# Performance work log

Hardware: AMD Instinct MI355X
Metric: run time of the kernel (lower is better)

The kernel has to match this reference:

```python
import jax, jax.numpy as jnp
import numpy as np

D_MODEL = 1024
D_STATE = 16
D_CONV = 4
EXPAND = 2
HEADDIM = 64
NGROUPS = 1
D_INNER = EXPAND * D_MODEL            # 2048
NHEADS = D_INNER // HEADDIM           # 32
CONV_DIM = D_INNER + 2 * NGROUPS * D_STATE   # 2080
D_IN_PROJ = 2 * D_INNER + 2 * NGROUPS * D_STATE + NHEADS  # 4160
EPS = 1e-5
BATCH, SEQLEN = 4, 2048


def setup_inputs() -> dict:
    key = jax.random.key(0)
    ks = jax.random.split(key, 8)
    x = jax.random.normal(ks[0], (BATCH, SEQLEN, D_MODEL), jnp.float32)
    W_in = jax.random.normal(ks[1], (D_MODEL, D_IN_PROJ), jnp.float32) * 0.02
    conv_w = jax.random.normal(ks[2], (CONV_DIM, D_CONV), jnp.float32) * 0.2
    conv_b = jnp.zeros((CONV_DIM,), jnp.float32)
    # dt_bias = inverse softplus of dt drawn in [1e-3, 1e-1] (mamba_ssm init)
    dt = jax.random.uniform(ks[3], (NHEADS,), jnp.float32, 0.001, 0.1)
    dt_bias = jnp.log(jnp.expm1(dt))
    A_log = jnp.log(jax.random.uniform(ks[4], (NHEADS,), jnp.float32, 1.0, 16.0))
    D_param = jnp.ones((NHEADS,), jnp.float32)
    norm_w = jnp.ones((D_INNER,), jnp.float32)
    W_out = jax.random.normal(ks[5], (D_INNER, D_MODEL), jnp.float32) * 0.02
    layer_scale = jnp.full((D_MODEL,), 1e-4, jnp.float32)
    return dict(x=x, W_in=W_in, conv_w=conv_w, conv_b=conv_b, dt_bias=dt_bias,
                A_log=A_log, D_param=D_param, norm_w=norm_w, W_out=W_out,
                layer_scale=layer_scale)


def _silu(v):
    return v * jax.nn.sigmoid(v)


def _mamba2(x, W_in, conv_w, conv_b, dt_bias, A_log, D_param, norm_w, W_out):
    b, l, _ = x.shape
    zxbcdt = x @ W_in                                  # (b, l, d_in_proj)
    z = zxbcdt[..., :D_INNER]                          # gate
    xBC = zxbcdt[..., D_INNER:D_INNER + CONV_DIM]
    dt = jax.nn.softplus(zxbcdt[..., D_INNER + CONV_DIM:] + dt_bias)  # (b, l, h)
    # causal depthwise conv1d (kernel D_CONV) + SiLU
    xp = jnp.pad(xBC, ((0, 0), (D_CONV - 1, 0), (0, 0)))
    conv = sum(xp[:, k:k + l, :] * conv_w[:, k] for k in range(D_CONV)) + conv_b
    xBC = _silu(conv)
    xs = xBC[..., :D_INNER].reshape(b, l, NHEADS, HEADDIM)  # (b, l, h, p)
    Bm = xBC[..., D_INNER:D_INNER + D_STATE]                # (b, l, n), ngroups=1
    Cm = xBC[..., D_INNER + D_STATE:]                       # (b, l, n)
    A = -jnp.exp(A_log)                                     # (h,)
    dA = jnp.exp(dt * A)                                    # (b, l, h)
    dtx = dt[..., None] * xs                                # (b, l, h, p)

    def step(h, inp):
        dA_t, dtx_t, B_t, C_t = inp
        # h: (b, h, p, n)
        h = h * dA_t[..., None, None] + dtx_t[..., None] * B_t[:, None, None, :]
        y = jnp.einsum('bhpn,bn->bhp', h, C_t)
        return h, y

    h0 = jnp.zeros((b, NHEADS, HEADDIM, D_STATE), x.dtype)
    _, ys = jax.lax.scan(step, h0, (dA.transpose(1, 0, 2), dtx.transpose(1, 0, 2, 3),
                                    Bm.transpose(1, 0, 2), Cm.transpose(1, 0, 2)))
    y = ys.transpose(1, 0, 2, 3) + D_param[None, None, :, None] * xs  # (b, l, h, p)
    y = y.reshape(b, l, D_INNER)
    # gated RMSNorm (norm_before_gate=False): gate first, then rmsnorm
    y = y * _silu(z)
    y = y * jax.lax.rsqrt(jnp.mean(y * y, axis=-1, keepdims=True) + EPS) * norm_w
    return y @ W_out


def reference(x, W_in, conv_w, conv_b, dt_bias, A_log, D_param, norm_w, W_out, layer_scale):
    # dropout is identity (eval / p=0)
    return x + _mamba2(x, W_in, conv_w, conv_b, dt_bias, A_log, D_param, norm_w, W_out) * layer_scale
```

## Files before the change

### kernel.cpp

```cpp
#include <hip/hip_runtime.h>
#include <hip/hip_bf16.h>

#define D_MODEL   1024
#define D_STATE   16
#define D_CONV    4
#define HEADDIM   64
#define NHEADS    32
#define D_INNER   2048
#define CONV_DIM  2080
#define D_IN_PROJ 4160
#define NPAD      4224
#define BATCH     4
#define SEQLEN    2048
#define MROWS     (BATCH*SEQLEN)
#define QCHUNK    64
#define NCHUNK    (SEQLEN/QCHUNK)
#define DT_COL    (2*D_INNER + 2*D_STATE)

#define WSCALE    16.f
#define YSCALE    64.f

__device__ __forceinline__ unsigned short f2b(float f) {
    union { float f; unsigned int u; } v; v.f = f;
    unsigned int r = (v.u + 0x7FFFu + ((v.u >> 16) & 1u)) >> 16;
    return (unsigned short)r;
}
__device__ __forceinline__ float b2f(unsigned short h) {
    union { unsigned int u; float f; } v; v.u = ((unsigned int)h) << 16;
    return v.f;
}
__device__ __forceinline__ unsigned char f2fp8(float f) {
    return (unsigned char)(__builtin_amdgcn_cvt_pk_fp8_f32(f, 0.f, 0, false) & 0xFF);
}

typedef __attribute__((ext_vector_type(8))) short bf16x8;
typedef __attribute__((ext_vector_type(4))) float f32x4;
typedef __attribute__((ext_vector_type(4))) int   i32x4;
typedef __attribute__((ext_vector_type(8))) int   i32x8;

__device__ __forceinline__ i32x8 cat8(i32x4 a, i32x4 b) {
    i32x8 r;
    r[0] = a[0]; r[1] = a[1]; r[2] = a[2]; r[3] = a[3];
    r[4] = b[0]; r[5] = b[1]; r[6] = b[2]; r[7] = b[3];
    return r;
}

__device__ __forceinline__ void async_copy16b(const unsigned char* g, unsigned char* l) {
    __builtin_amdgcn_global_load_lds(
        (const __attribute__((address_space(1))) void*)g,
        (__attribute__((address_space(3))) void*)l, 16, 0, 0);
}

__global__ void cast_f32_fp8(const float* __restrict__ in, unsigned char* __restrict__ out, int n) {
    int i = (blockIdx.x * blockDim.x + threadIdx.x) * 4;
    if (i >= n) return;
    float4 v = *(const float4*)&in[i];
    int p = __builtin_amdgcn_cvt_pk_fp8_f32(v.x, v.y, 0, false);
    p = __builtin_amdgcn_cvt_pk_fp8_f32(v.z, v.w, p, true);
    *(unsigned int*)&out[i] = (unsigned int)p;
}

__global__ void transpose_both(const float* __restrict__ W_in, unsigned char* __restrict__ winT,
                               const float* __restrict__ W_out, unsigned char* __restrict__ woutT,
                               const float* __restrict__ norm_w) {
    __shared__ float tile[64][65];
    int bid = blockIdx.x;
    const float* W; unsigned char* WT; const float* kscale;
    int K, N, bx, by;
    if (bid < 1056) { W = W_in;  WT = winT;  kscale = nullptr; K = 1024; N = 4160; bx = bid % 66; by = bid / 66; }
    else { bid -= 1056; W = W_out; WT = woutT; kscale = norm_w; K = 2048; N = 1024; bx = bid % 16; by = bid / 16; }
    int n0 = bx * 64, k0 = by * 64;
    int tx = threadIdx.x & 63, ty = threadIdx.x >> 6;
    #pragma unroll
    for (int i = 0; i < 16; i++) {
        int r = ty * 16 + i;
        int n = n0 + tx;
        float v = (n < N) ? W[(size_t)(k0 + r) * N + n] : 0.f;
        tile[r][tx] = v;
    }
    __syncthreads();
    float ks = WSCALE * (kscale ? kscale[k0 + tx] : 1.f);
    #pragma unroll
    for (int i = 0; i < 16; i++) {
        int r = ty * 16 + i;
        WT[(size_t)(n0 + r) * K + k0 + tx] = f2fp8(tile[tx][r] * ks);
    }
}

template <int EPI>
__global__ __launch_bounds__(256)
void gemm_fp8(const unsigned char* __restrict__ A, const unsigned char* __restrict__ B,
              int K, int N, unsigned short* __restrict__ Cb,
              float* __restrict__ Cf, const float* __restrict__ xres,
              const float* __restrict__ ls, const float* __restrict__ rs) {
    __shared__ unsigned char lds_a[128 * 128];
    __shared__ unsigned char lds_b[128 * 128];
    const int tid  = threadIdx.x;
    const int wave = tid >> 6;
    const int lane = tid & 63;
    const int bid = blockIdx.x;
    const int xcd = bid & 7, g = bid >> 3;
    const int bm = xcd * 8 + (g & 7);
    const int bn = g >> 3;
    const int wm = wave >> 1, wn = wave & 1;

    f32x4 acc[4][4];
    #pragma unroll
    for (int i = 0; i < 4; i++)
        #pragma unroll
        for (int j = 0; j < 4; j++) acc[i][j] = (f32x4){0.f, 0.f, 0.f, 0.f};

    const int srow = lane >> 3;
    const int sseg = (lane & 7) ^ srow;
    const unsigned char* gA0 = A + (size_t)(bm * 128 + wave * 8 + srow) * K + sseg * 16;
    const unsigned char* gB0 = B + (size_t)(bn * 128 + wave * 8 + srow) * K + sseg * 16;
    const int ldsbase = wave * 8 * 128;

    const int lm = lane & 15, q = lane >> 4;

    for (int k0 = 0; k0 < K; k0 += 128) {
        #pragma unroll
        for (int j = 0; j < 4; j++) {
            async_copy16b(gA0 + k0 + (size_t)(j * 32) * K, &lds_a[ldsbase + j * 32 * 128]);
            async_copy16b(gB0 + k0 + (size_t)(j * 32) * K, &lds_b[ldsbase + j * 32 * 128]);
        }
        __syncthreads();

        i32x8 af[4], bfr[4];
        #pragma unroll
        for (int i = 0; i < 4; i++) {
            int r = wm * 64 + i * 16 + lm;
            int s0 = ((2 * q) ^ (r & 7)) * 16, s1 = ((2 * q + 1) ^ (r & 7)) * 16;
            af[i] = cat8(*(const i32x4*)&lds_a[r * 128 + s0],
                         *(const i32x4*)&lds_a[r * 128 + s1]);
        }
        #pragma unroll
        for (int j = 0; j < 4; j++) {
            int r = wn * 64 + j * 16 + lm;
            int s0 = ((2 * q) ^ (r & 7)) * 16, s1 = ((2 * q + 1) ^ (r & 7)) * 16;
            bfr[j] = cat8(*(const i32x4*)&lds_b[r * 128 + s0],
                          *(const i32x4*)&lds_b[r * 128 + s1]);
        }
        #pragma unroll
        for (int i = 0; i < 4; i++)
            #pragma unroll
            for (int j = 0; j < 4; j++)
                acc[i][j] = __builtin_amdgcn_mfma_scale_f32_16x16x128_f8f6f4(
                    af[i], bfr[j], acc[i][j], 0, 0,
                    0, 0x7F7F7F7F, 0, 0x7F7F7F7F);
        __syncthreads();
    }

    const int row0 = bm * 128 + wm * 64;
    const int col0 = bn * 128 + wn * 64;
    const int lq = (lane >> 4) * 4;
    #pragma unroll
    for (int i = 0; i < 4; i++) {
        #pragma unroll
        for (int j = 0; j < 4; j++) {
            #pragma unroll
            for (int r = 0; r < 4; r++) {
                int gr = row0 + i * 16 + lq + r;
                int gc = col0 + j * 16 + lm;
                float v = acc[i][j][r];
                if (EPI == 0) {
                    Cb[(size_t)gr * N + gc] = f2b(v * (1.f / WSCALE));
                } else {
                    size_t idx = (size_t)gr * 1024 + gc;
                    Cf[idx] = xres[idx] + v * ls[gc] * rs[gr] * (1.f / (WSCALE * YSCALE));
                }
            }
        }
    }
}

__global__ __launch_bounds__(256)
void ssd_hcomp(const unsigned short* __restrict__ zx, const float* __restrict__ dt_bias,
               const float* __restrict__ conv_w, const float* __restrict__ conv_b,
               const float* __restrict__ A_log,
               float* __restrict__ hbuf, float* __restrict__ pbuf) {
    __shared__ unsigned short sXraw[67 * 64];
    __shared__ unsigned short sBraw[67 * 32];
    __shared__ unsigned short sXT[64 * 72];
    __shared__ unsigned short sBwT[16 * 72];
    __shared__ float sdt[64], scd[64];

    const int blk = blockIdx.x;
    const int c  = blk & 31;
    const int h  = (blk >> 5) & 31;
    const int b  = blk >> 10;
    const int bh = blk >> 5;
    const int row0 = b * SEQLEN + c * QCHUNK;
    const int batch0 = b * SEQLEN;

    const int t    = threadIdx.x;
    const int w    = t >> 6;
    const int lane = t & 63;
    const int lm   = lane & 15;
    const int lq8  = (lane >> 4) * 8;
    const int lq4  = (lane >> 4) * 4;
    const float Ah = -__expf(A_log[h]);

    for (int i = t; i < 536; i += 256) {
        int r = i >> 3, seg = i & 7;
        int gr = row0 - 3 + r;
        int4 v = (gr >= batch0) ? *(const int4*)&zx[(size_t)gr * NPAD + D_INNER + h * 64 + seg * 8]
                                : (int4){0, 0, 0, 0};
        *(int4*)&sXraw[r * 64 + seg * 8] = v;
    }
    for (int i = t; i < 268; i += 256) {
        int r = i >> 2, seg = i & 3;
        int gr = row0 - 3 + r;
        int4 v = (gr >= batch0) ? *(const int4*)&zx[(size_t)gr * NPAD + 2 * D_INNER + seg * 8]
                                : (int4){0, 0, 0, 0};
        *(int4*)&sBraw[r * 32 + seg * 8] = v;
    }
    if (t < 64) {
        float raw = b2f(zx[(size_t)(row0 + t) * NPAD + DT_COL + h]) + dt_bias[h];
        float dtv = (raw > 20.f) ? raw : log1pf(__expf(raw));
        float v = dtv;
        #pragma unroll
        for (int o = 1; o < 64; o <<= 1) {
            float u = __shfl_up(v, o, 64);
            if (t >= o) v += u;
        }
        sdt[t] = dtv;
        scd[t] = v;
        if (t == 63) pbuf[bh * NCHUNK + c] = __expf(Ah * v);
    }
    __syncthreads();

    {
        const int p = t & 63, sblk = (t >> 6) * 16;
        const int ch = h * 64 + p;
        const float cw0 = conv_w[ch * 4 + 0], cw1 = conv_w[ch * 4 + 1];
        const float cw2 = conv_w[ch * 4 + 2], cw3 = conv_w[ch * 4 + 3];
        const float cb = conv_b[ch];
        #pragma unroll
        for (int i = 0; i < 16; i++) {
            int s = sblk + i;
            float acc = cb + cw0 * b2f(sXraw[s * 64 + p]) + cw1 * b2f(sXraw[(s + 1) * 64 + p])
                           + cw2 * b2f(sXraw[(s + 2) * 64 + p]) + cw3 * b2f(sXraw[(s + 3) * 64 + p]);
            float sv = acc / (1.f + __expf(-acc));
            sXT[p * 72 + s] = f2b(sv);
        }
    }
    {
        const int n = t & 15, s0 = (t >> 4) * 4;
        const int ch = D_INNER + n;
        const float cw0 = conv_w[ch * 4 + 0], cw1 = conv_w[ch * 4 + 1];
        const float cw2 = conv_w[ch * 4 + 2], cw3 = conv_w[ch * 4 + 3];
        const float cb = conv_b[ch];
        const float cdl = scd[63];
        #pragma unroll
        for (int i = 0; i < 4; i++) {
            int s = s0 + i;
            float acc = cb + cw0 * b2f(sBraw[s * 32 + n]) + cw1 * b2f(sBraw[(s + 1) * 32 + n])
                           + cw2 * b2f(sBraw[(s + 2) * 32 + n]) + cw3 * b2f(sBraw[(s + 3) * 32 + n]);
            float sv = acc / (1.f + __expf(-acc));
            float wgt = sdt[s] * __expf(Ah * (cdl - scd[s]));
            sBwT[n * 72 + s] = f2b(sv * wgt);
        }
    }
    __syncthreads();

    f32x4 hacc = (f32x4){0.f, 0.f, 0.f, 0.f};
    #pragma unroll
    for (int ks = 0; ks < 2; ks++) {
        bf16x8 af = *(const bf16x8*)&sBwT[lm * 72 + ks * 32 + lq8];
        bf16x8 bf_ = *(const bf16x8*)&sXT[(w * 16 + lm) * 72 + ks * 32 + lq8];
        hacc = __builtin_amdgcn_mfma_f32_16x16x32_bf16(af, bf_, hacc, 0, 0, 0);
    }
    #pragma unroll
    for (int r = 0; r < 4; r++)
        hbuf[(size_t)(bh * NCHUNK + c) * 1024 + (lq4 + r) * 64 + (w * 16 + lm)] = hacc[r];
}

__global__ __launch_bounds__(1024)
void ssd_state_scan(float* __restrict__ hbuf, const float* __restrict__ pbuf) {
    int bh = blockIdx.x;
    int t = threadIdx.x;
    __shared__ float sP[NCHUNK];
    if (t < NCHUNK) sP[t] = pbuf[bh * NCHUNK + t];
    __syncthreads();
    size_t base = (size_t)bh * NCHUNK * 1024 + t;
    float v[NCHUNK];
    #pragma unroll
    for (int c = 0; c < NCHUNK; c++) v[c] = hbuf[base + (size_t)c * 1024];
    float carry = 0.f;
    #pragma unroll
    for (int c = 0; c < NCHUNK; c++) {
        float tmp = v[c];
        v[c] = carry;
        carry = tmp + sP[c] * carry;
    }
    #pragma unroll
    for (int c = 0; c < NCHUNK; c++) hbuf[base + (size_t)c * 1024] = v[c];
}

__global__ __launch_bounds__(256)
void ssd_yfused(const unsigned short* __restrict__ zx, const float* __restrict__ dt_bias,
                const float* __restrict__ conv_w, const float* __restrict__ conv_b,
                const float* __restrict__ A_log, const float* __restrict__ D_param,
                const float* __restrict__ hbuf,
                unsigned char* __restrict__ y, float* __restrict__ ssq) {
    __shared__ unsigned short sXraw[67 * 64];
    __shared__ unsigned short sBCraw[67 * 32];
    __shared__ unsigned short sB[64 * 32];
    __shared__ unsigned short sC[64 * 32];
    __shared__ unsigned short sXT[64 * 72];
    __shared__ unsigned short sM[64 * 72];
    __shared__ unsigned short sHT[64 * 40];
    __shared__ float sdt[64], scd[64], sSc[64];

    const int blk = blockIdx.x;
    const int c  = blk & 31;
    const int h  = (blk >> 5) & 31;
    const int b  = blk >> 10;
    const int bh = blk >> 5;
    const int row0 = b * SEQLEN + c * QCHUNK;
    const int batch0 = b * SEQLEN;

    const int t    = threadIdx.x;
    const int w    = t >> 6;
    const int lane = t & 63;
    const int lm   = lane & 15;
    const int lq8  = (lane >> 4) * 8;
    const int lq4  = (lane >> 4) * 4;
    const float Ah = -__expf(A_log[h]);

    for (int i = t; i < 536; i += 256) {
        int r = i >> 3, seg = i & 7;
        int gr = row0 - 3 + r;
        int4 v = (gr >= batch0) ? *(const int4*)&zx[(size_t)gr * NPAD + D_INNER + h * 64 + seg * 8]
                                : (int4){0, 0, 0, 0};
        *(int4*)&sXraw[r * 64 + seg * 8] = v;
    }
    for (int i = t; i < 268; i += 256) {
        int r = i >> 2, seg = i & 3;
        int gr = row0 - 3 + r;
        int4 v = (gr >= batch0) ? *(const int4*)&zx[(size_t)gr * NPAD + 2 * D_INNER + seg * 8]
                                : (int4){0, 0, 0, 0};
        *(int4*)&sBCraw[r * 32 + seg * 8] = v;
    }
    {
        size_t hb = (size_t)(bh * NCHUNK + c) * 1024 + (size_t)t * 4;
        float4 hv = *(const float4*)&hbuf[hb];
        int n = t >> 4;
        int p0 = (t * 4) & 63;
        sHT[(p0 + 0) * 40 + n] = f2b(hv.x);
        sHT[(p0 + 1) * 40 + n] = f2b(hv.y);
        sHT[(p0 + 2) * 40 + n] = f2b(hv.z);
        sHT[(p0 + 3) * 40 + n] = f2b(hv.w);
    }
    if (t < 64) {
        float raw = b2f(zx[(size_t)(row0 + t) * NPAD + DT_COL + h]) + dt_bias[h];
        float dtv = (raw > 20.f) ? raw : log1pf(__expf(raw));
        float v = dtv;
        #pragma unroll
        for (int o = 1; o < 64; o <<= 1) {
            float u = __shfl_up(v, o, 64);
            if (t >= o) v += u;
        }
        sdt[t] = dtv;
        scd[t] = v;
        sSc[t] = __expf(Ah * v);
    } else if (t < 128) {
        int tt = t - 64;
        *(int4*)&sHT[tt * 40 + 16] = (int4){0, 0, 0, 0};
        *(int4*)&sHT[tt * 40 + 24] = (int4){0, 0, 0, 0};
    }
    __syncthreads();

    {
        const int p = t & 63, sblk = (t >> 6) * 16;
        const int ch = h * 64 + p;
        const float cw0 = conv_w[ch * 4 + 0], cw1 = conv_w[ch * 4 + 1];
        const float cw2 = conv_w[ch * 4 + 2], cw3 = conv_w[ch * 4 + 3];
        const float cb = conv_b[ch];
        #pragma unroll
        for (int i = 0; i < 16; i++) {
            int s = sblk + i;
            float acc = cb + cw0 * b2f(sXraw[s * 64 + p]) + cw1 * b2f(sXraw[(s + 1) * 64 + p])
                           + cw2 * b2f(sXraw[(s + 2) * 64 + p]) + cw3 * b2f(sXraw[(s + 3) * 64 + p]);
            float sv = acc / (1.f + __expf(-acc));
            sXT[p * 72 + s] = f2b(sv);
        }
    }
    {
        const int ch32 = t & 31, s0 = (t >> 5) * 8;
        const int ch = D_INNER + ch32;
        const float cw0 = conv_w[ch * 4 + 0], cw1 = conv_w[ch * 4 + 1];
        const float cw2 = conv_w[ch * 4 + 2], cw3 = conv_w[ch * 4 + 3];
        const float cb = conv_b[ch];
        unsigned short* dst = (ch32 < 16) ? &sB[ch32] : &sC[ch32 - 16];
        #pragma unroll
        for (int i = 0; i < 8; i++) {
            int s = s0 + i;
            float acc = cb + cw0 * b2f(sBCraw[s * 32 + ch32]) + cw1 * b2f(sBCraw[(s + 1) * 32 + ch32])
                           + cw2 * b2f(sBCraw[(s + 2) * 32 + ch32]) + cw3 * b2f(sBCraw[(s + 3) * 32 + ch32]);
            float sv = acc / (1.f + __expf(-acc));
            dst[s * 32] = f2b(sv);
        }
    }
    if (t < 64) {
        *(int4*)&sB[t * 32 + 16] = (int4){0, 0, 0, 0};
        *(int4*)&sB[t * 32 + 24] = (int4){0, 0, 0, 0};
        *(int4*)&sC[t * 32 + 16] = (int4){0, 0, 0, 0};
        *(int4*)&sC[t * 32 + 24] = (int4){0, 0, 0, 0};
    }
    __syncthreads();

    f32x4 sacc[4];
    {
        bf16x8 cfrag = *(const bf16x8*)&sC[(w * 16 + lm) * 32 + lq8];
        #pragma unroll
        for (int sb = 0; sb < 4; sb++) {
            if (sb <= w) {
                bf16x8 bfrag = *(const bf16x8*)&sB[(sb * 16 + lm) * 32 + lq8];
                sacc[sb] = __builtin_amdgcn_mfma_f32_16x16x32_bf16(
                    cfrag, bfrag, (f32x4){0.f, 0.f, 0.f, 0.f}, 0, 0, 0);
            }
        }
    }
    #pragma unroll
    for (int sb = 0; sb < 4; sb++) {
        int sp = sb * 16 + lm;
        if (sb > w) {
            #pragma unroll
            for (int r = 0; r < 4; r++) sM[(w * 16 + lq4 + r) * 72 + sp] = 0;
        } else {
            float dts = sdt[sp], cds = scd[sp];
            #pragma unroll
            for (int r = 0; r < 4; r++) {
                int tp = w * 16 + lq4 + r;
                float m = 0.f;
                if (sb < w || sp <= tp)
                    m = sacc[sb][r] * dts * __expf(Ah * (scd[tp] - cds));
                sM[tp * 72 + sp] = f2b(m);
            }
        }
    }

    f32x4 yacc[4];
    #pragma unroll
    for (int pb = 0; pb < 4; pb++) yacc[pb] = (f32x4){0.f, 0.f, 0.f, 0.f};
    #pragma unroll
    for (int ks = 0; ks < 2; ks++) {
        if (ks == 1 && w < 2) continue;
        bf16x8 af = *(const bf16x8*)&sM[(w * 16 + lm) * 72 + ks * 32 + lq8];
        #pragma unroll
        for (int pb = 0; pb < 4; pb++) {
            bf16x8 bf_ = *(const bf16x8*)&sXT[(pb * 16 + lm) * 72 + ks * 32 + lq8];
            yacc[pb] = __builtin_amdgcn_mfma_f32_16x16x32_bf16(af, bf_, yacc[pb], 0, 0, 0);
        }
    }
    f32x4 acc2[4];
    {
        bf16x8 cf2 = *(const bf16x8*)&sC[(w * 16 + lm) * 32 + lq8];
        #pragma unroll
        for (int pb = 0; pb < 4; pb++) {
            bf16x8 hf = *(const bf16x8*)&sHT[(pb * 16 + lm) * 40 + lq8];
            acc2[pb] = __builtin_amdgcn_mfma_f32_16x16x32_bf16(
                cf2, hf, (f32x4){0.f, 0.f, 0.f, 0.f}, 0, 0, 0);
        }
    }

    const float Dh = D_param[h];
    #pragma unroll
    for (int r = 0; r < 4; r++) {
        const int tp = w * 16 + lq4 + r;
        const size_t zrow = (size_t)(row0 + tp) * NPAD + h * 64;
        const size_t yrow = (size_t)(row0 + tp) * D_INNER + h * 64;
        float ssr = 0.f;
        #pragma unroll
        for (int pb = 0; pb < 4; pb++) {
            int pp = pb * 16 + lm;
            float xv = b2f(sXT[pp * 72 + tp]);
            float val = yacc[pb][r] + sSc[tp] * acc2[pb][r] + Dh * xv;
            float zv = b2f(zx[zrow + pp]);
            float yg = val * (zv / (1.f + __expf(-zv)));
            ssr += yg * yg;
            y[yrow + pp] = f2fp8(yg * YSCALE);
        }
        ssr += __shfl_xor(ssr, 1, 16);
        ssr += __shfl_xor(ssr, 2, 16);
        ssr += __shfl_xor(ssr, 4, 16);
        ssr += __shfl_xor(ssr, 8, 16);
        if (lm == 0)
            ssq[(size_t)(row0 + tp) * NHEADS + h] = ssr;
    }
}

__global__ __launch_bounds__(256)
void rowscale_kernel(const float* __restrict__ ssq, float* __restrict__ rs) {
    int row = blockIdx.x * 256 + threadIdx.x;
    const float4* p = (const float4*)&ssq[(size_t)row * NHEADS];
    float s = 0.f;
    #pragma unroll
    for (int i = 0; i < 8; i++) {
        float4 v = p[i];
        s += v.x + v.y + v.z + v.w;
    }
    rs[row] = rsqrtf(s * (1.f / D_INNER) + 1e-5f);
}

extern "C" void kernel_launch(void* const* d_in, const int* in_sizes, int n_in,
                              void* d_out, int out_size, void* d_ws, size_t ws_size,
                              hipStream_t stream) {
    const float* x        = (const float*)d_in[0];
    const float* W_in     = (const float*)d_in[1];
    const float* conv_w   = (const float*)d_in[2];
    const float* conv_b   = (const float*)d_in[3];
    const float* dt_bias  = (const float*)d_in[4];
    const float* A_log    = (const float*)d_in[5];
    const float* D_param  = (const float*)d_in[6];
    const float* norm_w   = (const float*)d_in[7];
    const float* W_out    = (const float*)d_in[8];
    const float* ls       = (const float*)d_in[9];
    float* out = (float*)d_out;

    char* ws = (char*)d_ws;
    size_t off = 0;
    unsigned char*  x_f8  = (unsigned char*)(ws + off);  off += (size_t)MROWS * D_MODEL;
    unsigned char*  winT  = (unsigned char*)(ws + off);  off += (size_t)NPAD * D_MODEL;
    unsigned char*  woutT = (unsigned char*)(ws + off);  off += (size_t)D_MODEL * D_INNER;
    unsigned short* zx    = (unsigned short*)(ws + off); off += (size_t)MROWS * NPAD * 2;
    float*          pbuf  = (float*)(ws + off);          off += (size_t)BATCH * NHEADS * NCHUNK * 4;
    unsigned char*  yb    = (unsigned char*)(ws + off);  off += (size_t)MROWS * D_INNER;
    float*          ssq   = (float*)(ws + off);          off += (size_t)MROWS * NHEADS * 4;
    float*          rsb   = (float*)(ws + off);          off += (size_t)MROWS * 4;
    float*          hbuf  = (float*)(ws + off);          off += (size_t)BATCH * NHEADS * NCHUNK * 1024 * 4;

    cast_f32_fp8<<<(MROWS * D_MODEL) / 1024, 256, 0, stream>>>(x, x_f8, MROWS * D_MODEL);
    transpose_both<<<1568, 256, 0, stream>>>(W_in, winT, W_out, woutT, norm_w);
    gemm_fp8<0><<<(NPAD / 128) * 64, 256, 0, stream>>>(
        x_f8, winT, D_MODEL, NPAD, zx, nullptr, nullptr, nullptr, nullptr);
    ssd_hcomp<<<BATCH * NHEADS * NCHUNK, 256, 0, stream>>>(
        zx, dt_bias, conv_w, conv_b, A_log, hbuf, pbuf);
    ssd_state_scan<<<BATCH * NHEADS, 1024, 0, stream>>>(hbuf, pbuf);
    ssd_yfused<<<BATCH * NHEADS * NCHUNK, 256, 0, stream>>>(
        zx, dt_bias, conv_w, conv_b, A_log, D_param, hbuf, yb, ssq);
    rowscale_kernel<<<MROWS / 256, 256, 0, stream>>>(ssq, rsb);
    gemm_fp8<1><<<(D_MODEL / 128) * 64, 256, 0, stream>>>(
        yb, woutT, D_INNER, D_MODEL, nullptr, out, x, ls, rsb);
}
```

Measured before the change: 276.5 us.

## Reuse conv and dt results from hcomp in yfused via global buffers

ssd_hcomp now writes the post-conv SiLU x (already transposed), the B/C conv outputs and the dt, cumsum and decay scalars to workspace buffers, and ssd_yfused reads them instead of recomputing the causal conv, softplus and prefix scan. The D skip term is folded into the diagonal of the intra-chunk matrix, z is staged through shared memory with coalesced loads, and the conv loops reuse a register sliding window. This removes duplicated conv and exp work and the halo loads in the second kernel. The cost is extra global writes and reads of about 32 MB of bf16 x data plus small side buffers, and folding D into bf16 M adds some rounding.

```diff
diff --git a/kernel.cpp b/kernel.cpp
--- a/kernel.cpp
+++ b/kernel.cpp
@@ -178,10 +178,13 @@
 void ssd_hcomp(const unsigned short* __restrict__ zx, const float* __restrict__ dt_bias,
                const float* __restrict__ conv_w, const float* __restrict__ conv_b,
                const float* __restrict__ A_log,
-               float* __restrict__ hbuf, float* __restrict__ pbuf) {
+               float* __restrict__ hbuf, float* __restrict__ pbuf,
+               unsigned short* __restrict__ xTg, unsigned short* __restrict__ bcg,
+               float* __restrict__ scA) {
     __shared__ unsigned short sXraw[67 * 64];
-    __shared__ unsigned short sBraw[67 * 32];
+    __shared__ unsigned short sBCraw[67 * 32];
     __shared__ unsigned short sXT[64 * 72];
+    __shared__ unsigned short sBC[64 * 32];
     __shared__ unsigned short sBwT[16 * 72];
     __shared__ float sdt[64], scd[64];
 
@@ -213,7 +216,7 @@
         int gr = row0 - 3 + r;
         int4 v = (gr >= batch0) ? *(const int4*)&zx[(size_t)gr * NPAD + 2 * D_INNER + seg * 8]
                                 : (int4){0, 0, 0, 0};
-        *(int4*)&sBraw[r * 32 + seg * 8] = v;
+        *(int4*)&sBCraw[r * 32 + seg * 8] = v;
     }
     if (t < 64) {
         float raw = b2f(zx[(size_t)(row0 + t) * NPAD + DT_COL + h]) + dt_bias[h];
@@ -226,40 +229,51 @@
         }
         sdt[t] = dtv;
         scd[t] = v;
-        if (t == 63) pbuf[bh * NCHUNK + c] = __expf(Ah * v);
+        float sc = __expf(Ah * v);
+        float* scrow = &scA[(size_t)(bh * NCHUNK + c) * 192];
+        scrow[t] = dtv; scrow[64 + t] = v; scrow[128 + t] = sc;
+        if (t == 63) pbuf[bh * NCHUNK + c] = sc;
     }
     __syncthreads();
 
     {
         const int p = t & 63, sblk = (t >> 6) * 16;
         const int ch = h * 64 + p;
-        const float cw0 = conv_w[ch * 4 + 0], cw1 = conv_w[ch * 4 + 1];
-        const float cw2 = conv_w[ch * 4 + 2], cw3 = conv_w[ch * 4 + 3];
+        const float4 cw = *(const float4*)&conv_w[ch * 4];
         const float cb = conv_b[ch];
+        float x0 = b2f(sXraw[(sblk + 0) * 64 + p]);
+        float x1 = b2f(sXraw[(sblk + 1) * 64 + p]);
+        float x2 = b2f(sXraw[(sblk + 2) * 64 + p]);
         #pragma unroll
         for (int i = 0; i < 16; i++) {
-            int s = sblk + i;
-            float acc = cb + cw0 * b2f(sXraw[s * 64 + p]) + cw1 * b2f(sXraw[(s + 1) * 64 + p])
-                           + cw2 * b2f(sXraw[(s + 2) * 64 + p]) + cw3 * b2f(sXraw[(s + 3) * 64 + p]);
+            float x3 = b2f(sXraw[(sblk + i + 3) * 64 + p]);
+            float acc = cb + cw.x * x0 + cw.y * x1 + cw.z * x2 + cw.w * x3;
             float sv = acc / (1.f + __expf(-acc));
-            sXT[p * 72 + s] = f2b(sv);
+            sXT[p * 72 + sblk + i] = f2b(sv);
+            x0 = x1; x1 = x2; x2 = x3;
         }
     }
     {
-        const int n = t & 15, s0 = (t >> 4) * 4;
-        const int ch = D_INNER + n;
-        const float cw0 = conv_w[ch * 4 + 0], cw1 = conv_w[ch * 4 + 1];
-        const float cw2 = conv_w[ch * 4 + 2], cw3 = conv_w[ch * 4 + 3];
+        const int ch32 = t & 31, s0 = (t >> 5) * 8;
+        const int ch = D_INNER + ch32;
+        const float4 cw = *(const float4*)&conv_w[ch * 4];
         const float cb = conv_b[ch];
         const float cdl = scd[63];
-        #pragma unroll
-        for (int i = 0; i < 4; i++) {
+        float x0 = b2f(sBCraw[(s0 + 0) * 32 + ch32]);
+        float x1 = b2f(sBCraw[(s0 + 1) * 32 + ch32]);
+        float x2 = b2f(sBCraw[(s0 + 2) * 32 + ch32]);
+        #pragma unroll
+        for (int i = 0; i < 8; i++) {
             int s = s0 + i;
-            float acc = cb + cw0 * b2f(sBraw[s * 32 + n]) + cw1 * b2f(sBraw[(s + 1) * 32 + n])
-                           + cw2 * b2f(sBraw[(s + 2) * 32 + n]) + cw3 * b2f(sBraw[(s + 3) * 32 + n]);
+            float x3 = b2f(sBCraw[(s + 3) * 32 + ch32]);
+            float acc = cb + cw.x * x0 + cw.y * x1 + cw.z * x2 + cw.w * x3;
             float sv = acc / (1.f + __expf(-acc));
-            float wgt = sdt[s] * __expf(Ah * (cdl - scd[s]));
-            sBwT[n * 72 + s] = f2b(sv * wgt);
+            sBC[s * 32 + ch32] = f2b(sv);
+            if (ch32 < 16) {
+                float wgt = sdt[s] * __expf(Ah * (cdl - scd[s]));
+                sBwT[ch32 * 72 + s] = f2b(sv * wgt);
+            }
+            x0 = x1; x1 = x2; x2 = x3;
         }
     }
     __syncthreads();
@@ -274,6 +288,19 @@
     #pragma unroll
     for (int r = 0; r < 4; r++)
         hbuf[(size_t)(bh * NCHUNK + c) * 1024 + (lq4 + r) * 64 + (w * 16 + lm)] = hacc[r];
+
+    #pragma unroll
+    for (int it = 0; it < 2; it++) {
+        int idx = t + it * 256;
+        int p = idx >> 3, seg = idx & 7;
+        *(int4*)&xTg[(size_t)(bh * 64 + p) * SEQLEN + c * 64 + seg * 8] =
+            *(const int4*)&sXT[p * 72 + seg * 8];
+    }
+    if (h == 0) {
+        int s = t >> 2, seg = t & 3;
+        *(int4*)&bcg[(size_t)(b * SEQLEN + c * 64 + s) * 32 + seg * 8] =
+            *(const int4*)&sBC[s * 32 + seg * 8];
+    }
 }
 
 __global__ __launch_bounds__(1024)
@@ -299,17 +326,17 @@
 }
 
 __global__ __launch_bounds__(256)
-void ssd_yfused(const unsigned short* __restrict__ zx, const float* __restrict__ dt_bias,
-                const float* __restrict__ conv_w, const float* __restrict__ conv_b,
+void ssd_yfused(const unsigned short* __restrict__ zx,
+                const unsigned short* __restrict__ xTg, const unsigned short* __restrict__ bcg,
+                const float* __restrict__ scA,
                 const float* __restrict__ A_log, const float* __restrict__ D_param,
                 const float* __restrict__ hbuf,
                 unsigned char* __restrict__ y, float* __restrict__ ssq) {
-    __shared__ unsigned short sXraw[67 * 64];
-    __shared__ unsigned short sBCraw[67 * 32];
+    __shared__ unsigned short sXT[64 * 72];
+    __shared__ unsigned short sM[64 * 72];
     __shared__ unsigned short sB[64 * 32];
     __shared__ unsigned short sC[64 * 32];
-    __shared__ unsigned short sXT[64 * 72];
-    __shared__ unsigned short sM[64 * 72];
+    __shared__ unsigned short sZ[64 * 64];
     __shared__ unsigned short sHT[64 * 40];
     __shared__ float sdt[64], scd[64], sSc[64];
 
@@ -319,7 +346,6 @@
     const int b  = blk >> 10;
     const int bh = blk >> 5;
     const int row0 = b * SEQLEN + c * QCHUNK;
-    const int batch0 = b * SEQLEN;
 
     const int t    = threadIdx.x;
     const int w    = t >> 6;
@@ -329,19 +355,25 @@
     const int lq4  = (lane >> 4) * 4;
     const float Ah = -__expf(A_log[h]);
 
-    for (int i = t; i < 536; i += 256) {
-        int r = i >> 3, seg = i & 7;
-        int gr = row0 - 3 + r;
-        int4 v = (gr >= batch0) ? *(const int4*)&zx[(size_t)gr * NPAD + D_INNER + h * 64 + seg * 8]
-                                : (int4){0, 0, 0, 0};
-        *(int4*)&sXraw[r * 64 + seg * 8] = v;
-    }
-    for (int i = t; i < 268; i += 256) {
-        int r = i >> 2, seg = i & 3;
-        int gr = row0 - 3 + r;
-        int4 v = (gr >= batch0) ? *(const int4*)&zx[(size_t)gr * NPAD + 2 * D_INNER + seg * 8]
-                                : (int4){0, 0, 0, 0};
-        *(int4*)&sBCraw[r * 32 + seg * 8] = v;
+    #pragma unroll
+    for (int it = 0; it < 2; it++) {
+        int idx = t + it * 256;
+        int p = idx >> 3, seg = idx & 7;
+        *(int4*)&sXT[p * 72 + seg * 8] =
+            *(const int4*)&xTg[(size_t)(bh * 64 + p) * SEQLEN + c * 64 + seg * 8];
+    }
+    #pragma unroll
+    for (int it = 0; it < 2; it++) {
+        int idx = t + it * 256;
+        int s = idx >> 3, seg = idx & 7;
+        *(int4*)&sZ[s * 64 + seg * 8] =
+            *(const int4*)&zx[(size_t)(row0 + s) * NPAD + h * 64 + seg * 8];
+    }
+    {
+        int s = t >> 2, seg = t & 3;
+        int4 v = *(const int4*)&bcg[(size_t)(b * SEQLEN + c * 64 + s) * 32 + seg * 8];
+        if (seg < 2) *(int4*)&sB[s * 32 + seg * 8] = v;
+        else         *(int4*)&sC[s * 32 + (seg - 2) * 8] = v;
     }
     {
         size_t hb = (size_t)(bh * NCHUNK + c) * 1024 + (size_t)t * 4;
@@ -354,60 +386,18 @@
         sHT[(p0 + 3) * 40 + n] = f2b(hv.w);
     }
     if (t < 64) {
-        float raw = b2f(zx[(size_t)(row0 + t) * NPAD + DT_COL + h]) + dt_bias[h];
-        float dtv = (raw > 20.f) ? raw : log1pf(__expf(raw));
-        float v = dtv;
-        #pragma unroll
-        for (int o = 1; o < 64; o <<= 1) {
-            float u = __shfl_up(v, o, 64);
-            if (t >= o) v += u;
-        }
-        sdt[t] = dtv;
-        scd[t] = v;
-        sSc[t] = __expf(Ah * v);
-    } else if (t < 128) {
-        int tt = t - 64;
-        *(int4*)&sHT[tt * 40 + 16] = (int4){0, 0, 0, 0};
-        *(int4*)&sHT[tt * 40 + 24] = (int4){0, 0, 0, 0};
-    }
-    __syncthreads();
-
-    {
-        const int p = t & 63, sblk = (t >> 6) * 16;
-        const int ch = h * 64 + p;
-        const float cw0 = conv_w[ch * 4 + 0], cw1 = conv_w[ch * 4 + 1];
-        const float cw2 = conv_w[ch * 4 + 2], cw3 = conv_w[ch * 4 + 3];
-        const float cb = conv_b[ch];
-        #pragma unroll
-        for (int i = 0; i < 16; i++) {
-            int s = sblk + i;
-            float acc = cb + cw0 * b2f(sXraw[s * 64 + p]) + cw1 * b2f(sXraw[(s + 1) * 64 + p])
-                           + cw2 * b2f(sXraw[(s + 2) * 64 + p]) + cw3 * b2f(sXraw[(s + 3) * 64 + p]);
-            float sv = acc / (1.f + __expf(-acc));
-            sXT[p * 72 + s] = f2b(sv);
-        }
-    }
-    {
-        const int ch32 = t & 31, s0 = (t >> 5) * 8;
-        const int ch = D_INNER + ch32;
-        const float cw0 = conv_w[ch * 4 + 0], cw1 = conv_w[ch * 4 + 1];
-        const float cw2 = conv_w[ch * 4 + 2], cw3 = conv_w[ch * 4 + 3];
-        const float cb = conv_b[ch];
-        unsigned short* dst = (ch32 < 16) ? &sB[ch32] : &sC[ch32 - 16];
-        #pragma unroll
-        for (int i = 0; i < 8; i++) {
-            int s = s0 + i;
-            float acc = cb + cw0 * b2f(sBCraw[s * 32 + ch32]) + cw1 * b2f(sBCraw[(s + 1) * 32 + ch32])
-                           + cw2 * b2f(sBCraw[(s + 2) * 32 + ch32]) + cw3 * b2f(sBCraw[(s + 3) * 32 + ch32]);
-            float sv = acc / (1.f + __expf(-acc));
-            dst[s * 32] = f2b(sv);
-        }
-    }
-    if (t < 64) {
         *(int4*)&sB[t * 32 + 16] = (int4){0, 0, 0, 0};
         *(int4*)&sB[t * 32 + 24] = (int4){0, 0, 0, 0};
         *(int4*)&sC[t * 32 + 16] = (int4){0, 0, 0, 0};
         *(int4*)&sC[t * 32 + 24] = (int4){0, 0, 0, 0};
+        *(int4*)&sHT[t * 40 + 16] = (int4){0, 0, 0, 0};
+        *(int4*)&sHT[t * 40 + 24] = (int4){0, 0, 0, 0};
+    }
+    if (t < 192) {
+        float v = scA[(size_t)(bh * NCHUNK + c) * 192 + t];
+        if (t < 64) sdt[t] = v;
+        else if (t < 128) scd[t - 64] = v;
+        else sSc[t - 128] = v;
     }
     __syncthreads();
 
@@ -423,6 +413,7 @@
             }
         }
     }
+    const float Dh = D_param[h];
     #pragma unroll
     for (int sb = 0; sb < 4; sb++) {
         int sp = sb * 16 + lm;
@@ -435,8 +426,10 @@
             for (int r = 0; r < 4; r++) {
                 int tp = w * 16 + lq4 + r;
                 float m = 0.f;
-                if (sb < w || sp <= tp)
+                if (sb < w || sp <= tp) {
                     m = sacc[sb][r] * dts * __expf(Ah * (scd[tp] - cds));
+                    if (sp == tp) m += Dh;
+                }
                 sM[tp * 72 + sp] = f2b(m);
             }
         }
@@ -466,19 +459,16 @@
         }
     }
 
-    const float Dh = D_param[h];
     #pragma unroll
     for (int r = 0; r < 4; r++) {
         const int tp = w * 16 + lq4 + r;
-        const size_t zrow = (size_t)(row0 + tp) * NPAD + h * 64;
         const size_t yrow = (size_t)(row0 + tp) * D_INNER + h * 64;
         float ssr = 0.f;
         #pragma unroll
         for (int pb = 0; pb < 4; pb++) {
             int pp = pb * 16 + lm;
-            float xv = b2f(sXT[pp * 72 + tp]);
-            float val = yacc[pb][r] + sSc[tp] * acc2[pb][r] + Dh * xv;
-            float zv = b2f(zx[zrow + pp]);
+            float val = yacc[pb][r] + sSc[tp] * acc2[pb][r];
+            float zv = b2f(sZ[tp * 64 + pp]);
             float yg = val * (zv / (1.f + __expf(-zv)));
             ssr += yg * yg;
             y[yrow + pp] = f2fp8(yg * YSCALE);
@@ -531,16 +521,19 @@
     float*          ssq   = (float*)(ws + off);          off += (size_t)MROWS * NHEADS * 4;
     float*          rsb   = (float*)(ws + off);          off += (size_t)MROWS * 4;
     float*          hbuf  = (float*)(ws + off);          off += (size_t)BATCH * NHEADS * NCHUNK * 1024 * 4;
+    unsigned short* xTg   = (unsigned short*)(ws + off); off += (size_t)MROWS * D_INNER * 2;
+    unsigned short* bcg   = (unsigned short*)(ws + off); off += (size_t)MROWS * 32 * 2;
+    float*          scA   = (float*)(ws + off);          off += (size_t)BATCH * NHEADS * NCHUNK * 192 * 4;
 
     cast_f32_fp8<<<(MROWS * D_MODEL) / 1024, 256, 0, stream>>>(x, x_f8, MROWS * D_MODEL);
     transpose_both<<<1568, 256, 0, stream>>>(W_in, winT, W_out, woutT, norm_w);
     gemm_fp8<0><<<(NPAD / 128) * 64, 256, 0, stream>>>(
         x_f8, winT, D_MODEL, NPAD, zx, nullptr, nullptr, nullptr, nullptr);
     ssd_hcomp<<<BATCH * NHEADS * NCHUNK, 256, 0, stream>>>(
-        zx, dt_bias, conv_w, conv_b, A_log, hbuf, pbuf);
+        zx, dt_bias, conv_w, conv_b, A_log, hbuf, pbuf, xTg, bcg, scA);
     ssd_state_scan<<<BATCH * NHEADS, 1024, 0, stream>>>(hbuf, pbuf);
     ssd_yfused<<<BATCH * NHEADS * NCHUNK, 256, 0, stream>>>(
-        zx, dt_bias, conv_w, conv_b, A_log, D_param, hbuf, yb, ssq);
+        zx, xTg, bcg, scA, A_log, D_param, hbuf, yb, ssq);
     rowscale_kernel<<<MROWS / 256, 256, 0, stream>>>(ssq, rsb);
     gemm_fp8<1><<<(D_MODEL / 128) * 64, 256, 0, stream>>>(
         yb, woutT, D_INNER, D_MODEL, nullptr, out, x, ls, rsb);
```

Measured after the change: 269.0 us. 1.03x faster.
